# Optimization experiments

Measured on AMD Instinct MI355X. Metric: run time of the kernel, lower is better.

Reference implementation:

```python
import jax, jax.numpy as jnp
import numpy as np

B, T, D_IN = 64, 256, 256
H, N, W, R, D_OUT = 512, 128, 64, 4, 256
CTRL_IN = D_IN + R * W          # 512
IFACE = R * W + R + W + 1 + W + W + R * 3  # 465
EPS = 1e-8


def setup_inputs() -> dict:
    key = jax.random.key(0)
    ks = jax.random.split(key, 10)
    def lin(k, out_d, in_d):
        s = 1.0 / np.sqrt(in_d)
        return jax.random.uniform(k, (out_d, in_d), jnp.float32, -s, s)
    def vec(k, d, in_d):
        s = 1.0 / np.sqrt(in_d)
        return jax.random.uniform(k, (d,), jnp.float32, -s, s)
    return {
        'x': jax.random.normal(ks[0], (B, T, D_IN), jnp.float32),
        'W_ih': lin(ks[1], 4 * H, CTRL_IN),
        'W_hh': lin(ks[2], 4 * H, H),
        'b_ih': vec(ks[3], 4 * H, H),
        'b_hh': vec(ks[4], 4 * H, H),
        'W_int': lin(ks[5], IFACE, H),
        'b_int': vec(ks[6], IFACE, H),
        'W_out': lin(ks[7], D_OUT, H + R * W),
        'b_out': vec(ks[8], D_OUT, H + R * W),
    }


def _content_weights(mem, keys, strength):
    # mem: (b, n, w); keys: (b, r, w); strength: (b, r, 1) -> weights (b, r, n)
    dot = jnp.einsum('brw,bnw->brn', keys, mem)
    nm = jnp.maximum(jnp.linalg.norm(mem, axis=-1), EPS)      # (b, n)
    nk = jnp.maximum(jnp.linalg.norm(keys, axis=-1), EPS)     # (b, r)
    sim = dot / (nk[:, :, None] * nm[:, None, :])
    return jax.nn.softmax(strength * sim, axis=-1)


def reference(x, W_ih, W_hh, b_ih, b_hh, W_int, b_int, W_out, b_out):
    b = x.shape[0]

    def step(carry, x_t):
        h, c, mem, rv = carry
        ci = jnp.concatenate([x_t, rv.reshape(b, R * W)], axis=-1)
        gates = ci @ W_ih.T + b_ih + h @ W_hh.T + b_hh
        i_g, f_g, g_g, o_g = jnp.split(gates, 4, axis=-1)  # torch LSTM gate order
        c = jax.nn.sigmoid(f_g) * c + jax.nn.sigmoid(i_g) * jnp.tanh(g_g)
        h = jax.nn.sigmoid(o_g) * jnp.tanh(c)

        iface = h @ W_int.T + b_int
        idx = 0
        read_keys = iface[:, idx:idx + R * W].reshape(b, R, W); idx += R * W
        read_str = jax.nn.softplus(iface[:, idx:idx + R]) + 1.0; idx += R
        write_key = iface[:, idx:idx + W]; idx += W
        write_str = jax.nn.softplus(iface[:, idx:idx + 1]) + 1.0; idx += 1
        erase = jax.nn.sigmoid(iface[:, idx:idx + W]); idx += W
        write_vec = iface[:, idx:idx + W]; idx += W
        # read_modes are parsed in the original but never used -> skipped

        ww = _content_weights(mem, write_key[:, None, :], write_str[:, None, :])[:, 0, :]  # (b, n)
        mem = mem * (1.0 - ww[:, :, None] * erase[:, None, :]) + ww[:, :, None] * write_vec[:, None, :]

        rw = _content_weights(mem, read_keys, read_str[:, :, None])  # (b, r, n)
        rv = jnp.einsum('brn,bnw->brw', rw, mem)

        out = jnp.concatenate([h, rv.reshape(b, R * W)], axis=-1) @ W_out.T + b_out
        return (h, c, mem, rv), out

    init = (jnp.zeros((b, H), x.dtype), jnp.zeros((b, H), x.dtype),
            jnp.zeros((b, N, W), x.dtype), jnp.zeros((b, R, W), x.dtype))
    _, outs = jax.lax.scan(step, init, jnp.swapaxes(x, 0, 1))  # outs: (T, b, D_OUT)
    return outs[-1]  # return_sequence=False -> last timestep
```

## Files before the change

### kernel.cpp

```cpp
#include <hip/hip_runtime.h>
#include <math.h>

#define BB_   64
#define TT_   256
#define DIN_  256
#define HH_   512
#define NMEM_ 128
#define WWID_ 64
#define RR_   4
#define DOUT_ 256
#define CTRL_ 512
#define EPSV  1e-8f
#define NBLK  256
#define NTHR  512
#define OSTR  456
#define MPAD  65

__device__ __forceinline__ float sigm(float x){ return 1.f/(1.f+expf(-x)); }
__device__ __forceinline__ float softp(float x){ return (x>20.f)? x : log1pf(expf(x)); }
__device__ __forceinline__ float wredsum(float v){
  #pragma unroll
  for (int o=32;o>0;o>>=1) v += __shfl_xor(v,o,64);
  return v;
}
__device__ __forceinline__ float wredmax(float v){
  #pragma unroll
  for (int o=32;o>0;o>>=1) v = fmaxf(v, __shfl_xor(v,o,64));
  return v;
}

__device__ __forceinline__ float2 cload2(const float* p){
  unsigned long long u = __hip_atomic_load((const unsigned long long*)p,
                          __ATOMIC_RELAXED, __HIP_MEMORY_SCOPE_AGENT);
  float2 r; __builtin_memcpy(&r, &u, 8); return r;
}
__device__ __forceinline__ void cstore2(float* p, float2 v){
  unsigned long long u; __builtin_memcpy(&u, &v, 8);
  __hip_atomic_store((unsigned long long*)p, u, __ATOMIC_RELAXED,
                     __HIP_MEMORY_SCOPE_AGENT);
}
__device__ __forceinline__ void cstore1(float* p, float v){
  unsigned u; __builtin_memcpy(&u, &v, 4);
  __hip_atomic_store((unsigned*)p, u, __ATOMIC_RELAXED, __HIP_MEMORY_SCOPE_AGENT);
}

__device__ __forceinline__ void gridbar(unsigned* bar, unsigned k)
{
  __syncthreads();
  if (threadIdx.x == 0) {
    const int g = blockIdx.x >> 3;
    unsigned a = __hip_atomic_fetch_add(bar + g*32, 1u, __ATOMIC_RELAXED,
                                        __HIP_MEMORY_SCOPE_AGENT);
    bool released = false;
    if (a == 8u*k - 1u) {
      unsigned r = __hip_atomic_fetch_add(bar + 1024, 1u, __ATOMIC_RELAXED,
                                          __HIP_MEMORY_SCOPE_AGENT);
      if (r == 32u*k - 1u) {
        __hip_atomic_store(bar + 1056, k, __ATOMIC_RELAXED,
                           __HIP_MEMORY_SCOPE_AGENT);
        released = true;
      }
    }
    if (!released) {
      while (__hip_atomic_load(bar + 1056, __ATOMIC_RELAXED,
                               __HIP_MEMORY_SCOPE_AGENT) < k)
        __builtin_amdgcn_s_sleep(1);
    }
  }
  __syncthreads();
}

__global__ void k_initbar(unsigned* bar){
  int i = blockIdx.x*256 + threadIdx.x;
  if (i < 1088)
    __hip_atomic_store(bar + i, 0u, __ATOMIC_RELAXED, __HIP_MEMORY_SCOPE_AGENT);
}

__global__ void k_prep_w(const float* __restrict__ Wint, float* __restrict__ WiT4){
  const int o  = blockIdx.x;
  const int kq = threadIdx.x;
  float4 v = *(const float4*)(Wint + (size_t)o*HH_ + 4*kq);
  *(float4*)(WiT4 + ((size_t)kq*OSTR + o)*4) = v;
}

struct Params {
  const float *x, *Wih, *Whh, *bih, *bhh, *bint, *Wout, *bout;
  float *out;
  float *xbuf;
  float *hp;
  float *rvp;
  float *WiT4;
  unsigned *bar;
};

union __align__(16) SMu {
  float redA[8][8][64];
  float redO[4][4][64];
  struct {
    float hS[HH_];
    float ifcS[OSTR];
    float kpk[WWID_][8];
    float dH[4][NMEM_];
    float qH[4][NMEM_];
    float nH[4][NMEM_];
    float drH[4][RR_][NMEM_];
    float wwS[NMEM_];
    float rwS[RR_][NMEM_];
    float rvH[8][64];
    float scal[8];
    float red2[8];
  } c;
};

__launch_bounds__(NTHR, 2)
__global__ void k_persist(Params p)
{
  __shared__ SMu sm;
  __shared__ float memS[NMEM_][MPAD];

  const int bi  = blockIdx.x;
  const int tid = threadIdx.x;
  const int b   = tid & 63;
  const int wv  = tid >> 6;
  const int j0  = bi*2;
  const int bb  = bi;

  float c_reg = 0.f;

  const float* ap_sel;
  const float* wb[8];
  int qbase;
  {
    const float* wsrc; int koff;
    if      (wv < 2) { wsrc = p.Wih; koff = wv*128;            qbase = wv*32; }
    else if (wv < 4) { wsrc = p.Wih; koff = 256 + (wv-2)*128;  qbase = (wv-2)*32; }
    else             { wsrc = p.Whh; koff = (wv-4)*128;        qbase = (wv-4)*32; }
    #pragma unroll
    for (int r = 0; r < 8; ++r)
      wb[r] = wsrc + (size_t)((r>>1)*HH_ + j0 + (r&1))*CTRL_ + koff;
    ap_sel = nullptr; (void)ap_sel;
  }

  float bsum[4];
  if (tid < 128) {
    const int j = j0 + (tid >> 6);
    #pragma unroll
    for (int g = 0; g < 4; ++g)
      bsum[g] = p.bih[g*HH_ + j] + p.bhh[g*HH_ + j];
  }
  float bintR = 0.f;
  if (bi < 64 && tid < 453) bintR = p.bint[tid];

  {
    const float2 zz = make_float2(0.f, 0.f);
    const int gt = bi*NTHR + tid;
    if      (gt < 16384) cstore2(p.hp  + 2*gt,         zz);
    else if (gt < 24576) cstore2(p.rvp + 2*(gt-16384), zz);
    if (bi < 64)
      for (int i = tid; i < NMEM_*MPAD; i += NTHR)
        ((float*)memS)[i] = 0.f;
    if (bi >= 64 && bi < 128 && tid < 64) {
      const int B = bi - 64;
      float4 v = *(const float4*)(p.x + (size_t)B*(TT_*DIN_) + 4*tid);
      float* d = p.xbuf + tid*256 + B*4;
      cstore2(d,   make_float2(v.x, v.y));
      cstore2(d+2, make_float2(v.z, v.w));
    }
  }
  unsigned bk = 1;
  gridbar(p.bar, bk);

  for (int t = 0; t < TT_; ++t) {
    const int cur = t & 1, nxt = cur ^ 1;
    const float* hR = p.hp + cur*32768;
    float*       hW = p.hp + nxt*32768;

    {
      const float* ap = (wv < 2) ? (p.xbuf + cur*16384)
                       : (wv < 4) ? p.rvp : hR;

      float acc[8];
      #pragma unroll
      for (int r = 0; r < 8; ++r) acc[r] = 0.f;

      #pragma unroll 4
      for (int kk = 0; kk < 32; ++kk) {
        const float* a8 = ap + (((qbase + kk) << 6) + b)*4;
        float2 alo = cload2(a8);
        float2 ahi = cload2(a8 + 2);
        #pragma unroll
        for (int r = 0; r < 8; ++r) {
          float4 w = *(const float4*)(wb[r] + (kk << 2));
          acc[r] += w.x*alo.x + w.y*alo.y + w.z*ahi.x + w.w*ahi.y;
        }
      }
      #pragma unroll
      for (int r = 0; r < 8; ++r) sm.redA[wv][r][b] = acc[r];
      __syncthreads();

      if (tid < 128) {
        const int jj = tid >> 6;
        const int j  = j0 + jj;
        float gs[4];
        #pragma unroll
        for (int g = 0; g < 4; ++g) {
          float s = bsum[g];
          #pragma unroll
          for (int w8 = 0; w8 < 8; ++w8) s += sm.redA[w8][g*2+jj][b];
          gs[g] = s;
        }
        float cn = sigm(gs[1])*c_reg + sigm(gs[0])*tanhf(gs[2]);
        c_reg = cn;
        float hn = sigm(gs[3])*tanhf(cn);
        cstore1(hW + (j>>2)*256 + b*4 + (j&3), hn);
      }
    }
    gridbar(p.bar, ++bk);

    if (bi < 64) {
      if (tid < 128) {
        const float* hsrc = hW + tid*256 + bb*4;
        float2 lo = cload2(hsrc), hi = cload2(hsrc + 2);
        sm.c.hS[4*tid]   = lo.x; sm.c.hS[4*tid+1] = lo.y;
        sm.c.hS[4*tid+2] = hi.x; sm.c.hS[4*tid+3] = hi.y;
      }
      __syncthreads();
      {
        const int o = (tid < 453) ? tid : 452;
        float acc = bintR;
        #pragma unroll 8
        for (int kq = 0; kq < 128; ++kq) {
          float4 w  = *(const float4*)(p.WiT4 + ((size_t)kq*OSTR + o)*4);
          float4 h4 = *(const float4*)&sm.c.hS[kq << 2];
          acc += w.x*h4.x + w.y*h4.y + w.z*h4.z + w.w*h4.w;
        }
        if (tid < 453) sm.c.ifcS[tid] = acc;
      }
      __syncthreads();

      if (tid < 64) {
        const int w = tid;
        float wk = sm.c.ifcS[260+w];
        float q0 = sm.c.ifcS[w],      q1 = sm.c.ifcS[64+w];
        float q2 = sm.c.ifcS[128+w],  q3 = sm.c.ifcS[192+w];
        float er  = sigm(sm.c.ifcS[325+w]);
        float wvc = sm.c.ifcS[389+w];
        sm.c.kpk[w][0]=wk; sm.c.kpk[w][1]=q0; sm.c.kpk[w][2]=q1; sm.c.kpk[w][3]=q2;
        sm.c.kpk[w][4]=q3; sm.c.kpk[w][5]=er; sm.c.kpk[w][6]=wvc; sm.c.kpk[w][7]=0.f;
        float s0 = wredsum(wk*wk);
        float s1 = wredsum(q0*q0);
        float s2 = wredsum(q1*q1);
        float s3 = wredsum(q2*q2);
        float s4 = wredsum(q3*q3);
        if (w == 0) {
          sm.c.scal[0] = fmaxf(sqrtf(s0), EPSV);
          sm.c.scal[1] = fmaxf(sqrtf(s1), EPSV);
          sm.c.scal[2] = fmaxf(sqrtf(s2), EPSV);
          sm.c.scal[3] = fmaxf(sqrtf(s3), EPSV);
          sm.c.scal[4] = fmaxf(sqrtf(s4), EPSV);
        }
      }
      __syncthreads();

      const int n  = tid & 127;
      const int wh = tid >> 7;

      {
        float dotw = 0.f, q = 0.f;
        const int w0 = wh*16;
        #pragma unroll
        for (int w = 0; w < 16; ++w) {
          float m = memS[n][w0+w];
          dotw += sm.c.kpk[w0+w][0]*m;
          q    += m*m;
        }
        sm.c.dH[wh][n] = dotw;
        sm.c.qH[wh][n] = q;
      }
      __syncthreads();

      float a_n = 0.f, e_n = 0.f;
      const float wstr = softp(sm.c.ifcS[324]) + 1.f;
      if (tid < 128) {
        float dot = sm.c.dH[0][n] + sm.c.dH[1][n] + sm.c.dH[2][n] + sm.c.dH[3][n];
        float q2  = sm.c.qH[0][n] + sm.c.qH[1][n] + sm.c.qH[2][n] + sm.c.qH[3][n];
        a_n = wstr * dot / (sm.c.scal[0] * fmaxf(sqrtf(q2), EPSV));
        float mx = wredmax(a_n);
        if ((tid & 63) == 0) sm.c.red2[tid>>6] = mx;
      }
      __syncthreads();
      if (tid < 128) {
        float mx = fmaxf(sm.c.red2[0], sm.c.red2[1]);
        e_n = expf(a_n - mx);
        float s = wredsum(e_n);
        if ((tid & 63) == 0) sm.c.red2[4 + (tid>>6)] = s;
      }
      __syncthreads();
      if (tid < 128)
        sm.c.wwS[n] = e_n / (sm.c.red2[4] + sm.c.red2[5]);
      __syncthreads();

      {
        float ww_n = sm.c.wwS[n];
        float nrm=0.f, d0=0.f, d1=0.f, d2=0.f, d3=0.f;
        const int w0 = wh*16;
        #pragma unroll
        for (int w = 0; w < 16; ++w) {
          float4 k0 = *(const float4*)&sm.c.kpk[w0+w][0];
          float4 k1 = *(const float4*)&sm.c.kpk[w0+w][4];
          float m  = memS[n][w0+w];
          float mn = m*(1.f - ww_n*k1.y) + ww_n*k1.z;
          memS[n][w0+w] = mn;
          nrm += mn*mn;
          d0 += k0.y*mn; d1 += k0.z*mn; d2 += k0.w*mn; d3 += k1.x*mn;
        }
        sm.c.nH[wh][n] = nrm;
        sm.c.drH[wh][0][n]=d0; sm.c.drH[wh][1][n]=d1;
        sm.c.drH[wh][2][n]=d2; sm.c.drH[wh][3][n]=d3;
      }
      __syncthreads();

      if (tid < 128) {
        float nrm = sm.c.nH[0][n] + sm.c.nH[1][n] + sm.c.nH[2][n] + sm.c.nH[3][n];
        float inm = 1.f / fmaxf(sqrtf(nrm), EPSV);
        #pragma unroll
        for (int r = 0; r < RR_; ++r) {
          float rstr = softp(sm.c.ifcS[256+r]) + 1.f;
          float dr = sm.c.drH[0][r][n] + sm.c.drH[1][r][n]
                   + sm.c.drH[2][r][n] + sm.c.drH[3][r][n];
          sm.c.rwS[r][n] = rstr * dr * inm / sm.c.scal[1+r];
        }
      }
      __syncthreads();

      if (tid < 256) {
        float v0 = sm.c.rwS[wv][b], v1 = sm.c.rwS[wv][b+64];
        float mx = wredmax(fmaxf(v0, v1));
        float e0 = expf(v0-mx), e1 = expf(v1-mx);
        float s  = wredsum(e0+e1);
        sm.c.rwS[wv][b]    = e0/s;
        sm.c.rwS[wv][b+64] = e1/s;
      }
      __syncthreads();

      {
        const int r  = wv >> 1;
        const int n0 = (wv & 1) * 64;
        float acc = 0.f;
        #pragma unroll 4
        for (int n2 = n0; n2 < n0 + 64; n2 += 4) {
          float4 r4 = *(const float4*)&sm.c.rwS[r][n2];
          acc += r4.x*memS[n2][b]   + r4.y*memS[n2+1][b]
               + r4.z*memS[n2+2][b] + r4.w*memS[n2+3][b];
        }
        sm.c.rvH[wv][b] = acc;
      }
      __syncthreads();
      if (tid < 256) {
        const int r = tid >> 6;
        float acc = sm.c.rvH[2*r][b] + sm.c.rvH[2*r+1][b];
        const int k = r*64 + b;
        cstore1(p.rvp + (k>>2)*256 + bb*4 + (k&3), acc);
      }
    } else if (bi < 128) {
      if (t+1 < TT_ && tid < 64) {
        const int B = bi - 64;
        float4 v = *(const float4*)(p.x + (size_t)B*(TT_*DIN_)
                                    + (size_t)(t+1)*DIN_ + 4*tid);
        float* d = p.xbuf + nxt*16384 + tid*256 + B*4;
        cstore2(d,   make_float2(v.x, v.y));
        cstore2(d+2, make_float2(v.z, v.w));
      }
    }
    gridbar(p.bar, ++bk);
  }

  if (bi < 64) {
    const int o0 = bi*4;
    if (tid < 256) {
      float acc[4] = {0.f, 0.f, 0.f, 0.f};
      #pragma unroll 4
      for (int kk = 0; kk < 48; ++kk) {
        const int k = wv*192 + kk*4;
        const float* a8 = (k < 512)
          ? (p.hp  + (((k    )>>2)*64 + b)*4)
          : (p.rvp + (((k-512)>>2)*64 + b)*4);
        float2 alo = cload2(a8);
        float2 ahi = cload2(a8 + 2);
        #pragma unroll
        for (int r = 0; r < 4; ++r) {
          float4 w = *(const float4*)(p.Wout + (size_t)(o0+r)*(HH_ + RR_*WWID_) + k);
          acc[r] += w.x*alo.x + w.y*alo.y + w.z*ahi.x + w.w*ahi.y;
        }
      }
      #pragma unroll
      for (int r = 0; r < 4; ++r) sm.redO[wv][r][b] = acc[r];
    }
    __syncthreads();
    if (tid < 64) {
      float4 o4;
      float* po = (float*)&o4;
      #pragma unroll
      for (int r = 0; r < 4; ++r)
        po[r] = sm.redO[0][r][b] + sm.redO[1][r][b] + sm.redO[2][r][b]
              + sm.redO[3][r][b] + p.bout[o0+r];
      *(float4*)(p.out + (size_t)b*DOUT_ + o0) = o4;
    }
  }
}

extern "C" void kernel_launch(void* const* d_in, const int* in_sizes, int n_in,
                              void* d_out, int out_size, void* d_ws, size_t ws_size,
                              hipStream_t stream)
{
  Params prm;
  prm.x    = (const float*)d_in[0];
  prm.Wih  = (const float*)d_in[1];
  prm.Whh  = (const float*)d_in[2];
  prm.bih  = (const float*)d_in[3];
  prm.bhh  = (const float*)d_in[4];
  const float* Wint = (const float*)d_in[5];
  prm.bint = (const float*)d_in[6];
  prm.Wout = (const float*)d_in[7];
  prm.bout = (const float*)d_in[8];
  prm.out  = (float*)d_out;

  float* ws = (float*)d_ws;
  size_t off = 0;
  prm.xbuf = ws + off; off += 2*16384;
  prm.hp   = ws + off; off += 2*32768;
  prm.rvp  = ws + off; off += 16384;
  prm.WiT4 = ws + off; off += (size_t)128*OSTR*4;
  prm.bar  = (unsigned*)(ws + off); off += 2048;

  k_prep_w<<<453, 128, 0, stream>>>(Wint, prm.WiT4);
  k_initbar<<<5, 256, 0, stream>>>(prm.bar);
  k_persist<<<NBLK, NTHR, 0, stream>>>(prm);
}
```

Baseline: 9.407 ms.

## Pre-transpose all timesteps of x up front and split the gate GEMV per wave

When the workspace is large enough, all of x is transposed into an interleaved layout during the prologue using an LDS tile. Each timestep can then read its x slice with plain float4 loads instead of blocks 64-127 staging it every step through coherent stores. The gate GEMV is restructured so every wave covers a slice of x, rv and h, rather than each wave owning one input. The interface dot product now uses four independent accumulators to shorten the dependency chain. The cost is a larger prologue and extra workspace, with a fallback to the old staging path when the workspace is too small.

```diff
diff --git a/kernel.cpp b/kernel.cpp
--- a/kernel.cpp
+++ b/kernel.cpp
@@ -90,12 +90,15 @@
   float *hp;
   float *rvp;
   float *WiT4;
+  float *xT;
   unsigned *bar;
+  int useXT;
 };
 
 union __align__(16) SMu {
   float redA[8][8][64];
   float redO[4][4][64];
+  float tile[64][65];
   struct {
     float hS[HH_];
     float ifcS[OSTR];
@@ -127,19 +130,10 @@
 
   float c_reg = 0.f;
 
-  const float* ap_sel;
-  const float* wb[8];
-  int qbase;
-  {
-    const float* wsrc; int koff;
-    if      (wv < 2) { wsrc = p.Wih; koff = wv*128;            qbase = wv*32; }
-    else if (wv < 4) { wsrc = p.Wih; koff = 256 + (wv-2)*128;  qbase = (wv-2)*32; }
-    else             { wsrc = p.Whh; koff = (wv-4)*128;        qbase = (wv-4)*32; }
-    #pragma unroll
-    for (int r = 0; r < 8; ++r)
-      wb[r] = wsrc + (size_t)((r>>1)*HH_ + j0 + (r&1))*CTRL_ + koff;
-    ap_sel = nullptr; (void)ap_sel;
-  }
+  int rowoff[8];
+  #pragma unroll
+  for (int r = 0; r < 8; ++r)
+    rowoff[r] = ((r>>1)*HH_ + j0 + (r&1))*CTRL_;
 
   float bsum[4];
   if (tid < 128) {
@@ -159,7 +153,28 @@
     if (bi < 64)
       for (int i = tid; i < NMEM_*MPAD; i += NTHR)
         ((float*)memS)[i] = 0.f;
-    if (bi >= 64 && bi < 128 && tid < 64) {
+    if (p.useXT) {
+      const int lane = tid & 63, rg = tid >> 6;
+      for (int q = 0; q < 4; ++q) {
+        const int k0 = q*64;
+        #pragma unroll
+        for (int i = 0; i < 8; ++i) {
+          const int brow = rg + i*8;
+          sm.tile[brow][lane] =
+            p.x[(size_t)brow*(TT_*DIN_) + (size_t)bi*DIN_ + k0 + lane];
+        }
+        __syncthreads();
+        #pragma unroll
+        for (int pp = 0; pp < 2; ++pp) {
+          const int idx = tid + 512*pp;
+          const int kql = idx >> 6, b2 = idx & 63;
+          float* d = p.xT + ((size_t)(bi*64 + q*16 + kql)*64 + b2)*4;
+          cstore2(d,   make_float2(sm.tile[b2][4*kql],   sm.tile[b2][4*kql+1]));
+          cstore2(d+2, make_float2(sm.tile[b2][4*kql+2], sm.tile[b2][4*kql+3]));
+        }
+        __syncthreads();
+      }
+    } else if (bi >= 64 && bi < 128 && tid < 64) {
       const int B = bi - 64;
       float4 v = *(const float4*)(p.x + (size_t)B*(TT_*DIN_) + 4*tid);
       float* d = p.xbuf + tid*256 + B*4;
@@ -176,22 +191,63 @@
     float*       hW = p.hp + nxt*32768;
 
     {
-      const float* ap = (wv < 2) ? (p.xbuf + cur*16384)
-                       : (wv < 4) ? p.rvp : hR;
-
       float acc[8];
       #pragma unroll
       for (int r = 0; r < 8; ++r) acc[r] = 0.f;
 
-      #pragma unroll 4
-      for (int kk = 0; kk < 32; ++kk) {
-        const float* a8 = ap + (((qbase + kk) << 6) + b)*4;
-        float2 alo = cload2(a8);
-        float2 ahi = cload2(a8 + 2);
-        #pragma unroll
-        for (int r = 0; r < 8; ++r) {
-          float4 w = *(const float4*)(wb[r] + (kk << 2));
-          acc[r] += w.x*alo.x + w.y*alo.y + w.z*ahi.x + w.w*ahi.y;
+      {
+        const float* wX = p.Wih + 32*wv;
+        if (p.useXT) {
+          const float* xsrc = p.xT + ((size_t)(t*64 + 8*wv)*64 + b)*4;
+          #pragma unroll
+          for (int kk = 0; kk < 8; ++kk) {
+            float4 a = *(const float4*)(xsrc + kk*256);
+            #pragma unroll
+            for (int r = 0; r < 8; ++r) {
+              float4 w = *(const float4*)(wX + rowoff[r] + (kk<<2));
+              acc[r] += w.x*a.x + w.y*a.y + w.z*a.z + w.w*a.w;
+            }
+          }
+        } else {
+          const float* xsrc = p.xbuf + cur*16384 + (8*wv*64 + b)*4;
+          #pragma unroll
+          for (int kk = 0; kk < 8; ++kk) {
+            float2 alo = cload2(xsrc + kk*256);
+            float2 ahi = cload2(xsrc + kk*256 + 2);
+            #pragma unroll
+            for (int r = 0; r < 8; ++r) {
+              float4 w = *(const float4*)(wX + rowoff[r] + (kk<<2));
+              acc[r] += w.x*alo.x + w.y*alo.y + w.z*ahi.x + w.w*ahi.y;
+            }
+          }
+        }
+      }
+      {
+        const float* wR = p.Wih + 256 + 32*wv;
+        const float* rsrc = p.rvp + (8*wv*64 + b)*4;
+        #pragma unroll
+        for (int kk = 0; kk < 8; ++kk) {
+          float2 alo = cload2(rsrc + kk*256);
+          float2 ahi = cload2(rsrc + kk*256 + 2);
+          #pragma unroll
+          for (int r = 0; r < 8; ++r) {
+            float4 w = *(const float4*)(wR + rowoff[r] + (kk<<2));
+            acc[r] += w.x*alo.x + w.y*alo.y + w.z*ahi.x + w.w*ahi.y;
+          }
+        }
+      }
+      {
+        const float* wH = p.Whh + 64*wv;
+        const float* hsrc = hR + (16*wv*64 + b)*4;
+        #pragma unroll
+        for (int kk = 0; kk < 16; ++kk) {
+          float2 alo = cload2(hsrc + kk*256);
+          float2 ahi = cload2(hsrc + kk*256 + 2);
+          #pragma unroll
+          for (int r = 0; r < 8; ++r) {
+            float4 w = *(const float4*)(wH + rowoff[r] + (kk<<2));
+            acc[r] += w.x*alo.x + w.y*alo.y + w.z*ahi.x + w.w*ahi.y;
+          }
         }
       }
       #pragma unroll
@@ -227,14 +283,14 @@
       __syncthreads();
       {
         const int o = (tid < 453) ? tid : 452;
-        float acc = bintR;
+        float a0 = bintR, a1 = 0.f, a2 = 0.f, a3 = 0.f;
         #pragma unroll 8
         for (int kq = 0; kq < 128; ++kq) {
           float4 w  = *(const float4*)(p.WiT4 + ((size_t)kq*OSTR + o)*4);
           float4 h4 = *(const float4*)&sm.c.hS[kq << 2];
-          acc += w.x*h4.x + w.y*h4.y + w.z*h4.z + w.w*h4.w;
-        }
-        if (tid < 453) sm.c.ifcS[tid] = acc;
+          a0 += w.x*h4.x; a1 += w.y*h4.y; a2 += w.z*h4.z; a3 += w.w*h4.w;
+        }
+        if (tid < 453) sm.c.ifcS[tid] = (a0 + a1) + (a2 + a3);
       }
       __syncthreads();
 
@@ -362,7 +418,7 @@
         const int k = r*64 + b;
         cstore1(p.rvp + (k>>2)*256 + bb*4 + (k&3), acc);
       }
-    } else if (bi < 128) {
+    } else if (!p.useXT && bi < 128) {
       if (t+1 < TT_ && tid < 64) {
         const int B = bi - 64;
         float4 v = *(const float4*)(p.x + (size_t)B*(TT_*DIN_)
@@ -432,6 +488,9 @@
   prm.rvp  = ws + off; off += 16384;
   prm.WiT4 = ws + off; off += (size_t)128*OSTR*4;
   prm.bar  = (unsigned*)(ws + off); off += 2048;
+  prm.xT   = ws + off;
+  const size_t needXT = (off + (size_t)TT_*64*64*4) * sizeof(float);
+  prm.useXT = (ws_size >= needXT) ? 1 : 0;
 
   k_prep_w<<<453, 128, 0, stream>>>(Wint, prm.WiT4);
   k_initbar<<<5, 256, 0, stream>>>(prm.bar);
```

Result: slower. 9.597 ms (+2.0%).

## Retile LSTM gate GEMM as 16 hidden units by 8 batches with LDS-staged activations

Applied to the files above, without the earlier changes.

The LSTM gate GEMM is repartitioned so that each block owns 16 hidden units across 8 batch rows instead of 2 hidden units across all 64 batches. Activations (x, rv, h) are staged through LDS, and x is now read directly from global memory, which removes the xbuf transpose buffer and the separate prefetch done by blocks 64-127. The goal is to cut per-block weight streaming and the cost of the cross-block activation reload. The interface matvec also gets split accumulators to raise ILP. In exchange there is a larger LDS footprint and more coherent loads per block.

```diff
diff --git a/kernel.cpp b/kernel.cpp
--- a/kernel.cpp
+++ b/kernel.cpp
@@ -86,7 +86,6 @@
 struct Params {
   const float *x, *Wih, *Whh, *bih, *bhh, *bint, *Wout, *bout;
   float *out;
-  float *xbuf;
   float *hp;
   float *rvp;
   float *WiT4;
@@ -94,7 +93,10 @@
 };
 
 union __align__(16) SMu {
-  float redA[8][8][64];
+  struct {
+    float4 actS[2048];
+    float  red[4][4][16][8];
+  } a;
   float redO[4][4][64];
   struct {
     float hS[HH_];
@@ -122,28 +124,30 @@
   const int tid = threadIdx.x;
   const int b   = tid & 63;
   const int wv  = tid >> 6;
-  const int j0  = bi*2;
+  const int rg  = bi & 31;
+  const int col = bi >> 5;
+  const int j0  = rg*16;
+  const int B0  = col*8;
   const int bb  = bi;
 
+  const int ksA = tid >> 7;
+  const int jlA = (tid >> 3) & 15;
+  const int blA = tid & 7;
+
   float c_reg = 0.f;
 
-  const float* ap_sel;
-  const float* wb[8];
-  int qbase;
+  const float* wbg[4];
   {
-    const float* wsrc; int koff;
-    if      (wv < 2) { wsrc = p.Wih; koff = wv*128;            qbase = wv*32; }
-    else if (wv < 4) { wsrc = p.Wih; koff = 256 + (wv-2)*128;  qbase = (wv-2)*32; }
-    else             { wsrc = p.Whh; koff = (wv-4)*128;        qbase = (wv-4)*32; }
+    const float* wsrc = (ksA < 2) ? p.Wih : p.Whh;
+    const int koff = (ksA & 1) * 256;
     #pragma unroll
-    for (int r = 0; r < 8; ++r)
-      wb[r] = wsrc + (size_t)((r>>1)*HH_ + j0 + (r&1))*CTRL_ + koff;
-    ap_sel = nullptr; (void)ap_sel;
+    for (int g = 0; g < 4; ++g)
+      wbg[g] = wsrc + (size_t)(g*HH_ + j0 + jlA)*CTRL_ + koff;
   }
 
   float bsum[4];
   if (tid < 128) {
-    const int j = j0 + (tid >> 6);
+    const int j = j0 + (tid >> 3);
     #pragma unroll
     for (int g = 0; g < 4; ++g)
       bsum[g] = p.bih[g*HH_ + j] + p.bhh[g*HH_ + j];
@@ -159,13 +163,6 @@
     if (bi < 64)
       for (int i = tid; i < NMEM_*MPAD; i += NTHR)
         ((float*)memS)[i] = 0.f;
-    if (bi >= 64 && bi < 128 && tid < 64) {
-      const int B = bi - 64;
-      float4 v = *(const float4*)(p.x + (size_t)B*(TT_*DIN_) + 4*tid);
-      float* d = p.xbuf + tid*256 + B*4;
-      cstore2(d,   make_float2(v.x, v.y));
-      cstore2(d+2, make_float2(v.z, v.w));
-    }
   }
   unsigned bk = 1;
   gridbar(p.bar, bk);
@@ -176,43 +173,59 @@
     float*       hW = p.hp + nxt*32768;
 
     {
-      const float* ap = (wv < 2) ? (p.xbuf + cur*16384)
-                       : (wv < 4) ? p.rvp : hR;
-
-      float acc[8];
       #pragma unroll
-      for (int r = 0; r < 8; ++r) acc[r] = 0.f;
-
+      for (int i = 0; i < 4; ++i) {
+        const int idx = tid + 512*i;
+        const int kq = idx >> 3, bl = idx & 7, bg = B0 + bl;
+        float4 v;
+        if (kq < 64) {
+          v = *(const float4*)(p.x + (size_t)bg*(TT_*DIN_)
+                               + (size_t)t*DIN_ + kq*4);
+        } else if (kq < 128) {
+          const float* s = p.rvp + (kq-64)*256 + bg*4;
+          float2 lo = cload2(s), hi = cload2(s + 2);
+          v = make_float4(lo.x, lo.y, hi.x, hi.y);
+        } else {
+          const float* s = hR + (kq-128)*256 + bg*4;
+          float2 lo = cload2(s), hi = cload2(s + 2);
+          v = make_float4(lo.x, lo.y, hi.x, hi.y);
+        }
+        sm.a.actS[idx] = v;
+      }
+      __syncthreads();
+
+      float4 ac[4];
+      #pragma unroll
+      for (int g = 0; g < 4; ++g) ac[g] = make_float4(0.f, 0.f, 0.f, 0.f);
+
+      const int kbase = ksA*64;
       #pragma unroll 4
-      for (int kk = 0; kk < 32; ++kk) {
-        const float* a8 = ap + (((qbase + kk) << 6) + b)*4;
-        float2 alo = cload2(a8);
-        float2 ahi = cload2(a8 + 2);
-        #pragma unroll
-        for (int r = 0; r < 8; ++r) {
-          float4 w = *(const float4*)(wb[r] + (kk << 2));
-          acc[r] += w.x*alo.x + w.y*alo.y + w.z*ahi.x + w.w*ahi.y;
+      for (int i = 0; i < 64; ++i) {
+        float4 a = sm.a.actS[(kbase + i)*8 + blA];
+        #pragma unroll
+        for (int g = 0; g < 4; ++g) {
+          float4 w = *(const float4*)(wbg[g] + (i << 2));
+          ac[g].x += w.x*a.x; ac[g].y += w.y*a.y;
+          ac[g].z += w.z*a.z; ac[g].w += w.w*a.w;
         }
       }
       #pragma unroll
-      for (int r = 0; r < 8; ++r) sm.redA[wv][r][b] = acc[r];
+      for (int g = 0; g < 4; ++g)
+        sm.a.red[ksA][g][jlA][blA] = (ac[g].x + ac[g].y) + (ac[g].z + ac[g].w);
       __syncthreads();
 
       if (tid < 128) {
-        const int jj = tid >> 6;
-        const int j  = j0 + jj;
+        const int jl = tid >> 3, bl = tid & 7;
         float gs[4];
         #pragma unroll
-        for (int g = 0; g < 4; ++g) {
-          float s = bsum[g];
-          #pragma unroll
-          for (int w8 = 0; w8 < 8; ++w8) s += sm.redA[w8][g*2+jj][b];
-          gs[g] = s;
-        }
+        for (int g = 0; g < 4; ++g)
+          gs[g] = sm.a.red[0][g][jl][bl] + sm.a.red[1][g][jl][bl]
+                + sm.a.red[2][g][jl][bl] + sm.a.red[3][g][jl][bl] + bsum[g];
         float cn = sigm(gs[1])*c_reg + sigm(gs[0])*tanhf(gs[2]);
         c_reg = cn;
         float hn = sigm(gs[3])*tanhf(cn);
-        cstore1(hW + (j>>2)*256 + b*4 + (j&3), hn);
+        const int j = j0 + jl, bg = B0 + bl;
+        cstore1(hW + (j>>2)*256 + bg*4 + (j&3), hn);
       }
     }
     gridbar(p.bar, ++bk);
@@ -227,14 +240,14 @@
       __syncthreads();
       {
         const int o = (tid < 453) ? tid : 452;
-        float acc = bintR;
+        float a0 = bintR, a1 = 0.f, a2 = 0.f, a3 = 0.f;
         #pragma unroll 8
         for (int kq = 0; kq < 128; ++kq) {
           float4 w  = *(const float4*)(p.WiT4 + ((size_t)kq*OSTR + o)*4);
           float4 h4 = *(const float4*)&sm.c.hS[kq << 2];
-          acc += w.x*h4.x + w.y*h4.y + w.z*h4.z + w.w*h4.w;
-        }
-        if (tid < 453) sm.c.ifcS[tid] = acc;
+          a0 += w.x*h4.x; a1 += w.y*h4.y; a2 += w.z*h4.z; a3 += w.w*h4.w;
+        }
+        if (tid < 453) sm.c.ifcS[tid] = (a0 + a1) + (a2 + a3);
       }
       __syncthreads();
 
@@ -362,15 +375,6 @@
         const int k = r*64 + b;
         cstore1(p.rvp + (k>>2)*256 + bb*4 + (k&3), acc);
       }
-    } else if (bi < 128) {
-      if (t+1 < TT_ && tid < 64) {
-        const int B = bi - 64;
-        float4 v = *(const float4*)(p.x + (size_t)B*(TT_*DIN_)
-                                    + (size_t)(t+1)*DIN_ + 4*tid);
-        float* d = p.xbuf + nxt*16384 + tid*256 + B*4;
-        cstore2(d,   make_float2(v.x, v.y));
-        cstore2(d+2, make_float2(v.z, v.w));
-      }
     }
     gridbar(p.bar, ++bk);
   }
@@ -427,7 +431,6 @@
 
   float* ws = (float*)d_ws;
   size_t off = 0;
-  prm.xbuf = ws + off; off += 2*16384;
   prm.hp   = ws + off; off += 2*32768;
   prm.rvp  = ws + off; off += 16384;
   prm.WiT4 = ws + off; off += (size_t)128*OSTR*4;
```

Result: faster. 8.562 ms (-9.0%).
